# Kernel optimization log

Measured on AMD Instinct MI355X. Metric: run time of the kernel, lower is better.

## Reference

```python
import jax, jax.numpy as jnp
import numpy as np
import math

B, T, N, D, L, H, TE = 4, 1024, 1024, 1024, 512, 16, 1024
HD = D // H  # 64


def layer_norm(x, g, b, eps=1e-5):
    m = jnp.mean(x, axis=-1, keepdims=True)
    v = jnp.var(x, axis=-1, keepdims=True)
    return (x - m) * jax.lax.rsqrt(v + eps) * g + b


def setup_inputs() -> dict:
    key = jax.random.key(0)
    ks = jax.random.split(key, 16)
    s = 0.02
    return {
        "x": jax.random.normal(ks[0], (B, T, D), jnp.float32),
        "xf": jax.random.normal(ks[1], (B, N, L), jnp.float32),
        "emb": jax.random.normal(ks[2], (B, TE), jnp.float32),
        "src_mask": jnp.ones((B, T, N), jnp.float32),
        # LayerNorms
        "ln_g": jnp.ones((D,), jnp.float32), "ln_b": jnp.zeros((D,), jnp.float32),
        "aln_g": jnp.ones((L,), jnp.float32), "aln_b": jnp.zeros((L,), jnp.float32),
        "n2_g": jnp.ones((D,), jnp.float32), "n2_b": jnp.zeros((D,), jnp.float32),
        # Q/K/V projections
        "Wq": jax.random.normal(ks[3], (D, D), jnp.float32) * s,
        "bq": jnp.zeros((D,), jnp.float32),
        "Wk": jax.random.normal(ks[4], (L, D), jnp.float32) * s,
        "bk": jnp.zeros((D,), jnp.float32),
        "Wv": jax.random.normal(ks[5], (L, D), jnp.float32) * s,
        "bv": jnp.zeros((D,), jnp.float32),
        # AdaLN: emb_layers Linear(TE, 2D); out Linear(D, D) (random, not zeroed, to exercise grads)
        "emb_W": jax.random.normal(ks[6], (TE, 2 * D), jnp.float32) * s,
        "emb_b": jnp.zeros((2 * D,), jnp.float32),
        "out_W": jax.random.normal(ks[7], (D, D), jnp.float32) * s,
        "out_b": jnp.zeros((D,), jnp.float32),
    }


def reference(x, xf, emb, src_mask, ln_g, ln_b, aln_g, aln_b, n2_g, n2_b,
              Wq, bq, Wk, bk, Wv, bv, emb_W, emb_b, out_W, out_b):
    xn = layer_norm(x, ln_g, ln_b)                      # B,T,D
    xfn = layer_norm(xf, aln_g, aln_b)                  # B,N,L
    q = (xn @ Wq + bq).reshape(B, T, H, HD)
    k = (xfn @ Wk + bk).reshape(B, N, H, HD)
    v = (xfn @ Wv + bv).reshape(B, N, H, HD)
    # scores: B,T,N,H; scaled by sqrt(head_dim)
    scores = jnp.einsum('bthd,bnhd->btnh', q, k) / math.sqrt(HD)
    scores = scores + (1.0 - src_mask[..., None]) * -100000.0
    weight = jax.nn.softmax(scores, axis=2)             # softmax over N
    y = jnp.einsum('btnh,bnhd->bthd', weight, v).reshape(B, T, D)
    # AdaLN proj_out
    emb_out = (jax.nn.silu(emb) @ emb_W + emb_b)[:, None, :]  # B,1,2D
    scale, shift = jnp.split(emb_out, 2, axis=2)
    h = layer_norm(y, n2_g, n2_b) * (1.0 + scale) + shift
    h = jax.nn.silu(h) @ out_W + out_b
    return x + h
```

## Files before the change

kernel.cpp:

```cpp
#include <hip/hip_runtime.h>

typedef __bf16 bf16;
typedef __bf16 bf16x4 __attribute__((ext_vector_type(4)));
typedef __bf16 bf16x8 __attribute__((ext_vector_type(8)));
typedef float f32x4 __attribute__((ext_vector_type(4)));

#define AS1C(p) ((const __attribute__((address_space(1))) void*)(p))
#define AS3(p)  ((__attribute__((address_space(3))) void*)(p))

__global__ __launch_bounds__(256) void transpose_cast(
    const float* __restrict__ in, bf16* __restrict__ out, int R, int C)
{
    __shared__ float tile[32][33];
    int tx = threadIdx.x & 31, ty = threadIdx.x >> 5;
    int r0 = blockIdx.y * 32, c0 = blockIdx.x * 32;
#pragma unroll
    for (int i = 0; i < 32; i += 8)
        tile[ty + i][tx] = in[(long)(r0 + ty + i) * C + c0 + tx];
    __syncthreads();
#pragma unroll
    for (int i = 0; i < 32; i += 8)
        out[(long)(c0 + ty + i) * R + r0 + tx] = (bf16)tile[tx][ty + i];
}

__global__ __launch_bounds__(256) void concat_bias(
    const float* __restrict__ b0, const float* __restrict__ b1, float* __restrict__ o)
{
    int c = blockIdx.x * 256 + threadIdx.x;
    o[c] = (c < 1024) ? b0[c] : b1[c - 1024];
}

template<int DIM, int NT>
__global__ __launch_bounds__(NT) void ln_to_bf16(
    const float* __restrict__ in, const float* __restrict__ g,
    const float* __restrict__ bb, bf16* __restrict__ out)
{
    constexpr int NW = NT / 64;
    long row = blockIdx.x;
    const float4* x4 = (const float4*)(in + row * DIM);
    float4 v = x4[threadIdx.x];
    float s = v.x + v.y + v.z + v.w;
    float s2 = v.x*v.x + v.y*v.y + v.z*v.z + v.w*v.w;
#pragma unroll
    for (int o = 32; o; o >>= 1) { s += __shfl_xor(s, o); s2 += __shfl_xor(s2, o); }
    __shared__ float red[2][NW];
    int w = threadIdx.x >> 6;
    if ((threadIdx.x & 63) == 0) { red[0][w] = s; red[1][w] = s2; }
    __syncthreads();
    s = 0.f; s2 = 0.f;
#pragma unroll
    for (int i = 0; i < NW; ++i) { s += red[0][i]; s2 += red[1][i]; }
    float mean = s * (1.f / DIM);
    float rstd = rsqrtf(s2 * (1.f / DIM) - mean * mean + 1e-5f);
    int c = threadIdx.x * 4;
    float4 gg = *(const float4*)(g + c);
    float4 bv = *(const float4*)(bb + c);
    bf16x4 ov;
    ov[0] = (bf16)((v.x - mean) * rstd * gg.x + bv.x);
    ov[1] = (bf16)((v.y - mean) * rstd * gg.y + bv.y);
    ov[2] = (bf16)((v.z - mean) * rstd * gg.z + bv.z);
    ov[3] = (bf16)((v.w - mean) * rstd * gg.w + bv.w);
    *(bf16x4*)(out + row * DIM + c) = ov;
}

__global__ __launch_bounds__(256) void mask_flags(
    const float* __restrict__ mask, unsigned char* __restrict__ flags)
{
    int blk = blockIdx.x;
    int b = blk >> 8, qt = (blk >> 4) & 15, kt = blk & 15;
    const float* src = mask + ((long)(b * 1024 + qt * 64 + (threadIdx.x >> 2))) * 1024
                     + kt * 64 + (threadIdx.x & 3) * 16;
    int ok = 1;
#pragma unroll
    for (int u = 0; u < 16; u += 4) {
        float4 v = *(const float4*)(src + u);
        ok &= (v.x == 1.f) & (v.y == 1.f) & (v.z == 1.f) & (v.w == 1.f);
    }
    ok = __syncthreads_and(ok);
    if (threadIdx.x == 0) flags[blk] = (unsigned char)ok;
}

__global__ __launch_bounds__(256) void adaln_gemm2(
    const float* __restrict__ emb, const float* __restrict__ W,
    const float* __restrict__ eb, float* __restrict__ emo)
{
    __shared__ float es[1024];
    __shared__ float part[4][64];
    int b = blockIdx.y, t = threadIdx.x;
    int kg = t >> 6, c = t & 63;
    int col = blockIdx.x * 64 + c;
    for (int i = t; i < 1024; i += 256) {
        float e = emb[b * 1024 + i];
        es[i] = e / (1.f + expf(-e));
    }
    __syncthreads();
    float acc = 0.f;
    const float* wp = W + (long)(kg * 256) * 2048 + col;
    const float* ep = es + kg * 256;
#pragma unroll 4
    for (int k = 0; k < 256; ++k) acc += ep[k] * wp[(long)k * 2048];
    part[kg][c] = acc;
    __syncthreads();
    if (t < 64) {
        int col0 = blockIdx.x * 64 + t;
        emo[b * 2048 + col0] = part[0][t] + part[1][t] + part[2][t] + part[3][t] + eb[col0];
    }
}

template<int OUT_MODE>
__global__ __launch_bounds__(256) void gemm64(
    const bf16* __restrict__ A, const bf16* __restrict__ Bt,
    const float* __restrict__ bias, const float* __restrict__ resid,
    void* __restrict__ outp, int M, int N, int K)
{
    __shared__ __align__(16) bf16 As[64 * 32];
    __shared__ __align__(16) bf16 Bs[128 * 32];
    const int t = threadIdx.x;
    const int wave = t >> 6, lane = t & 63;
    const int brow = blockIdx.y * 64, bcol = blockIdx.x * 128;
    const int wr = wave & 1, wc = wave >> 1;
    const int sr = lane >> 2, sc8 = (lane & 3) * 8;
    const bf16* aS  = A  + (long)(brow + wave * 16 + sr) * K + sc8;
    const bf16* bS0 = Bt + (long)(bcol + wave * 32 + sr) * K + sc8;
    const bf16* bS1 = bS0 + (long)16 * K;
    char* asw = (char*)As + wave * 1024;
    char* bsw = (char*)Bs + wave * 2048;
    const int fr = lane & 15, fc = (lane >> 4) * 8;
    f32x4 acc[2][4] = {};
    for (int k0 = 0; k0 < K; k0 += 32) {
        __syncthreads();
        __builtin_amdgcn_global_load_lds(AS1C(aS + k0),  AS3(asw), 16, 0, 0);
        __builtin_amdgcn_global_load_lds(AS1C(bS0 + k0), AS3(bsw), 16, 0, 0);
        __builtin_amdgcn_global_load_lds(AS1C(bS1 + k0), AS3(bsw + 1024), 16, 0, 0);
        __syncthreads();
        bf16x8 af[2], bfr[4];
#pragma unroll
        for (int m = 0; m < 2; ++m)
            af[m] = *(const bf16x8*)&As[(wr * 32 + m * 16 + fr) * 32 + fc];
#pragma unroll
        for (int n = 0; n < 4; ++n)
            bfr[n] = *(const bf16x8*)&Bs[(wc * 64 + n * 16 + fr) * 32 + fc];
        __builtin_amdgcn_s_setprio(1);
#pragma unroll
        for (int m = 0; m < 2; ++m)
#pragma unroll
            for (int n = 0; n < 4; ++n)
                acc[m][n] = __builtin_amdgcn_mfma_f32_16x16x32_bf16(af[m], bfr[n], acc[m][n], 0, 0, 0);
        __builtin_amdgcn_s_setprio(0);
    }
    const int er = (lane >> 4) * 4, ec = lane & 15;
    if constexpr (OUT_MODE == 0) {
        bf16* C = (bf16*)outp;
#pragma unroll
        for (int n = 0; n < 4; ++n) {
            int col = bcol + wc * 64 + n * 16 + ec;
            float bcv = bias[col];
#pragma unroll
            for (int m = 0; m < 2; ++m) {
                long rbase = (long)(brow + wr * 32 + m * 16 + er) * N + col;
#pragma unroll
                for (int j = 0; j < 4; ++j)
                    C[rbase + (long)j * N] = (bf16)(acc[m][n][j] + bcv);
            }
        }
    } else {
        float* C = (float*)outp;
#pragma unroll
        for (int n = 0; n < 4; ++n) {
            int col = bcol + wc * 64 + n * 16 + ec;
            float bcv = bias[col];
#pragma unroll
            for (int m = 0; m < 2; ++m) {
                long rbase = (long)(brow + wr * 32 + m * 16 + er) * N + col;
#pragma unroll
                for (int j = 0; j < 4; ++j) {
                    long idx = rbase + (long)j * N;
                    C[idx] = resid[idx] + acc[m][n][j] + bcv;
                }
            }
        }
    }
}

__global__ __launch_bounds__(256) void vtrans(
    const bf16* __restrict__ kvb, bf16* __restrict__ vt)
{
    __shared__ bf16 tile[64 * 72];
    int kvt = blockIdx.x, bh = blockIdx.y;
    int b = bh >> 4, h = bh & 15;
    int t = threadIdx.x;
    {
        int key = t >> 2, d0 = (t & 3) * 16;
        const bf16* src = kvb + (long)(b * 1024 + kvt * 64 + key) * 2048 + 1024 + h * 64 + d0;
        bf16x8 v0 = *(const bf16x8*)src;
        bf16x8 v1 = *(const bf16x8*)(src + 8);
        *(bf16x8*)&tile[key * 72 + d0] = v0;
        *(bf16x8*)&tile[key * 72 + d0 + 8] = v1;
    }
    __syncthreads();
    bf16* vtile = vt + ((long)(bh * 16 + kvt)) * 4096;
    int d = t >> 2;
    int phi = (d & 3) | (((d >> 3) & 1) << 2);
#pragma unroll
    for (int half = 0; half < 2; ++half) {
        int c = (t & 3) + half * 4;
        int key8 = 8 * (c ^ phi);
        bf16x8 w;
#pragma unroll
        for (int j = 0; j < 8; ++j) w[j] = tile[(key8 + j) * 72 + d];
        *(bf16x8*)&vtile[d * 64 + c * 8] = w;
    }
}

__global__ __launch_bounds__(256, 4) void flash2(
    const bf16* __restrict__ Q, const bf16* __restrict__ KV, const bf16* __restrict__ VT,
    const float* __restrict__ mask, const unsigned char* __restrict__ flags,
    bf16* __restrict__ Y)
{
    const int f = blockIdx.x;
    const int bh = f & 63;
    const int qt = f >> 6;
    const int b = bh >> 4, h = bh & 15;
    const int t = threadIdx.x, wave = t >> 6, lane = t & 63;
    const int la = lane >> 4, lb = lane & 15;

    __shared__ __align__(16) bf16 Ks[64 * 64];
    __shared__ __align__(16) bf16 Vs[64 * 64];

    const int qrow = qt * 64 + wave * 16;
    bf16x8 qf0, qf1;
    {
        const bf16* qp = Q + (long)(b * 1024 + qrow + lb) * 1024 + h * 64 + la * 8;
        qf0 = *(const bf16x8*)qp;
        qf1 = *(const bf16x8*)(qp + 32);
    }
    f32x4 o[4] = {};
    float m_run = -3e38f, l_run = 0.f;
    const float CL = 0.125f * 1.44269504f;

    const int srow = lane >> 3, sc = lane & 7;
    const int phiS = (srow & 3) | ((wave & 1) << 2);
    const bf16* kS = KV + (long)(b * 1024 + wave * 8 + srow) * 2048 + h * 64 + ((sc ^ phiS) * 8);
    const bf16* vS = VT + (long)(bh * 16) * 4096 + wave * 512 + lane * 8;
    char* kDst = (char*)Ks + wave * 1024;
    char* vDst = (char*)Vs + wave * 1024;

    const int phiK = (lb & 3) | (((lb >> 2) & 1) << 2);
    const int phiV = (lb & 3) | (((lb >> 3) & 1) << 2);
    const int rbase = (lb >> 2) * 8 + (lb & 3);
    const bf16* kf0 = &Ks[rbase * 64 + ((la ^ phiK) * 8)];
    const bf16* kf1 = &Ks[rbase * 64 + (((4 + la) ^ phiK) * 8)];
    const bf16* vf0 = &Vs[lb * 64 + ((la ^ phiV) * 8)];
    const bf16* vf1 = &Vs[lb * 64 + (((4 + la) ^ phiV) * 8)];
    const int rowoff[4] = {0, 2048, 256, 2304};

    const unsigned char* flagrow = flags + b * 256 + qt * 16;
    const float* mrow_p = mask + (long)(b * 1024 + qrow + lb) * 1024;

    for (int kv = 0; kv < 16; ++kv) {
        const int key0 = kv * 64;
        __syncthreads();
        __builtin_amdgcn_global_load_lds(AS1C(kS + (long)key0 * 2048),        AS3(kDst),        16, 0, 0);
        __builtin_amdgcn_global_load_lds(AS1C(kS + (long)(key0 + 32) * 2048), AS3(kDst + 4096), 16, 0, 0);
        __builtin_amdgcn_global_load_lds(AS1C(vS + kv * 4096),                AS3(vDst),        16, 0, 0);
        __builtin_amdgcn_global_load_lds(AS1C(vS + kv * 4096 + 2048),         AS3(vDst + 4096), 16, 0, 0);
        __syncthreads();

        f32x4 s[4] = {};
        __builtin_amdgcn_s_setprio(1);
#pragma unroll
        for (int n = 0; n < 4; ++n) {
            s[n] = __builtin_amdgcn_mfma_f32_16x16x32_bf16(*(const bf16x8*)(kf0 + rowoff[n]), qf0, s[n], 0, 0, 0);
            s[n] = __builtin_amdgcn_mfma_f32_16x16x32_bf16(*(const bf16x8*)(kf1 + rowoff[n]), qf1, s[n], 0, 0, 0);
        }
        __builtin_amdgcn_s_setprio(0);

        if (!flagrow[kv]) {
#pragma unroll
            for (int n = 0; n < 4; ++n)
#pragma unroll
                for (int r = 0; r < 4; ++r) {
                    int key = (n & 1) * 32 + la * 8 + (n >> 1) * 4 + r;
                    s[n][r] += (1.f - mrow_p[key0 + key]) * -800000.f;
                }
        }

        float t0 = fmaxf(fmaxf(s[0][0], s[0][1]), fmaxf(s[0][2], s[0][3]));
        float t1 = fmaxf(fmaxf(s[1][0], s[1][1]), fmaxf(s[1][2], s[1][3]));
        float t2 = fmaxf(fmaxf(s[2][0], s[2][1]), fmaxf(s[2][2], s[2][3]));
        float t3 = fmaxf(fmaxf(s[3][0], s[3][1]), fmaxf(s[3][2], s[3][3]));
        float tmax = fmaxf(fmaxf(t0, t1), fmaxf(t2, t3));
        tmax = fmaxf(tmax, __shfl_xor(tmax, 16));
        tmax = fmaxf(tmax, __shfl_xor(tmax, 32));
        float mnew = fmaxf(m_run, tmax);
        float al = exp2f((m_run - mnew) * CL);
        m_run = mnew;
        float p[4][4];
        float rsum = 0.f;
#pragma unroll
        for (int n = 0; n < 4; ++n)
#pragma unroll
            for (int r = 0; r < 4; ++r) {
                p[n][r] = exp2f((s[n][r] - mnew) * CL);
                rsum += p[n][r];
            }
        rsum += __shfl_xor(rsum, 16);
        rsum += __shfl_xor(rsum, 32);
        l_run = l_run * al + rsum;
#pragma unroll
        for (int d = 0; d < 4; ++d) o[d] *= al;

        bf16x8 pb0, pb1;
#pragma unroll
        for (int j = 0; j < 4; ++j) {
            pb0[j] = (bf16)p[0][j]; pb0[j + 4] = (bf16)p[2][j];
            pb1[j] = (bf16)p[1][j]; pb1[j + 4] = (bf16)p[3][j];
        }

        __builtin_amdgcn_s_setprio(1);
#pragma unroll
        for (int d = 0; d < 4; ++d) {
            o[d] = __builtin_amdgcn_mfma_f32_16x16x32_bf16(*(const bf16x8*)(vf0 + d * 1024), pb0, o[d], 0, 0, 0);
            o[d] = __builtin_amdgcn_mfma_f32_16x16x32_bf16(*(const bf16x8*)(vf1 + d * 1024), pb1, o[d], 0, 0, 0);
        }
        __builtin_amdgcn_s_setprio(0);
    }

    float inv = 1.f / l_run;
    bf16* yp = Y + (long)(b * 1024 + qrow + lb) * 1024 + h * 64 + la * 4;
#pragma unroll
    for (int d = 0; d < 4; ++d) {
        bf16x4 yv;
#pragma unroll
        for (int j = 0; j < 4; ++j) yv[j] = (bf16)(o[d][j] * inv);
        *(bf16x4*)(yp + d * 16) = yv;
    }
}

__global__ __launch_bounds__(256) void ln_mod_silu(
    const bf16* __restrict__ Yin, const float* __restrict__ g, const float* __restrict__ bb,
    const float* __restrict__ emo, bf16* __restrict__ act)
{
    long row = blockIdx.x;
    int b = (int)(row >> 10);
    const bf16* y = Yin + row * 1024;
    int c = threadIdx.x * 4;
    bf16x4 yv = *(const bf16x4*)(y + c);
    float v0 = (float)yv[0], v1 = (float)yv[1], v2 = (float)yv[2], v3 = (float)yv[3];
    float s = v0 + v1 + v2 + v3, s2 = v0*v0 + v1*v1 + v2*v2 + v3*v3;
#pragma unroll
    for (int o = 32; o; o >>= 1) { s += __shfl_xor(s, o); s2 += __shfl_xor(s2, o); }
    __shared__ float red[2][4];
    int w = threadIdx.x >> 6;
    if ((threadIdx.x & 63) == 0) { red[0][w] = s; red[1][w] = s2; }
    __syncthreads();
    s = red[0][0] + red[0][1] + red[0][2] + red[0][3];
    s2 = red[1][0] + red[1][1] + red[1][2] + red[1][3];
    float mean = s * (1.f / 1024.f);
    float rstd = rsqrtf(s2 * (1.f / 1024.f) - mean * mean + 1e-5f);
    float4 gg = *(const float4*)(g + c);
    float4 bv = *(const float4*)(bb + c);
    float4 scv = *(const float4*)(emo + b * 2048 + c);
    float4 shv = *(const float4*)(emo + b * 2048 + 1024 + c);
    float hv[4];
    hv[0] = ((v0 - mean) * rstd * gg.x + bv.x) * (1.f + scv.x) + shv.x;
    hv[1] = ((v1 - mean) * rstd * gg.y + bv.y) * (1.f + scv.y) + shv.y;
    hv[2] = ((v2 - mean) * rstd * gg.z + bv.z) * (1.f + scv.z) + shv.z;
    hv[3] = ((v3 - mean) * rstd * gg.w + bv.w) * (1.f + scv.w) + shv.w;
    bf16x4 ov;
#pragma unroll
    for (int j = 0; j < 4; ++j) ov[j] = (bf16)(hv[j] / (1.f + expf(-hv[j])));
    *(bf16x4*)(act + row * 1024 + c) = ov;
}

extern "C" void kernel_launch(void* const* d_in, const int* in_sizes, int n_in,
                              void* d_out, int out_size, void* d_ws, size_t ws_size,
                              hipStream_t stream)
{
    const float* x     = (const float*)d_in[0];
    const float* xf    = (const float*)d_in[1];
    const float* emb   = (const float*)d_in[2];
    const float* mask  = (const float*)d_in[3];
    const float* ln_g  = (const float*)d_in[4];
    const float* ln_b  = (const float*)d_in[5];
    const float* aln_g = (const float*)d_in[6];
    const float* aln_b = (const float*)d_in[7];
    const float* n2_g  = (const float*)d_in[8];
    const float* n2_b  = (const float*)d_in[9];
    const float* Wq    = (const float*)d_in[10];
    const float* bq    = (const float*)d_in[11];
    const float* Wk    = (const float*)d_in[12];
    const float* bk    = (const float*)d_in[13];
    const float* Wv    = (const float*)d_in[14];
    const float* bv    = (const float*)d_in[15];
    const float* emb_W = (const float*)d_in[16];
    const float* emb_b = (const float*)d_in[17];
    const float* out_W = (const float*)d_in[18];
    const float* out_b = (const float*)d_in[19];
    float* out = (float*)d_out;

    char* w = (char*)d_ws;
    bf16* xn   = (bf16*)w; w += (size_t)4096 * 1024 * 2;
    bf16* xfn  = (bf16*)w; w += (size_t)4096 * 512 * 2;
    bf16* WqT  = (bf16*)w; w += (size_t)1024 * 1024 * 2;
    bf16* WkvT = (bf16*)w; w += (size_t)2048 * 512 * 2;
    bf16* WoT  = (bf16*)w; w += (size_t)1024 * 1024 * 2;
    bf16* qb   = (bf16*)w; w += (size_t)4096 * 1024 * 2;
    bf16* kvb  = (bf16*)w; w += (size_t)4096 * 2048 * 2;
    bf16* yb   = (bf16*)w; w += (size_t)4096 * 1024 * 2;
    float* bkv = (float*)w; w += (size_t)2048 * 4;
    float* emo = (float*)w; w += (size_t)4 * 2048 * 4;
    unsigned char* flg = (unsigned char*)w;
    bf16* vt   = xn;
    bf16* actb = xn;

    transpose_cast<<<dim3(32, 32), 256, 0, stream>>>(Wq,    WqT, 1024, 1024);
    transpose_cast<<<dim3(32, 16), 256, 0, stream>>>(Wk,    WkvT, 512, 1024);
    transpose_cast<<<dim3(32, 16), 256, 0, stream>>>(Wv,    WkvT + (size_t)1024 * 512, 512, 1024);
    transpose_cast<<<dim3(32, 32), 256, 0, stream>>>(out_W, WoT, 1024, 1024);
    concat_bias<<<8, 256, 0, stream>>>(bk, bv, bkv);

    ln_to_bf16<1024, 256><<<4096, 256, 0, stream>>>(x,  ln_g,  ln_b,  xn);
    ln_to_bf16<512, 128><<<4096, 128, 0, stream>>>(xf, aln_g, aln_b, xfn);
    mask_flags<<<1024, 256, 0, stream>>>(mask, flg);
    adaln_gemm2<<<dim3(32, 4), 256, 0, stream>>>(emb, emb_W, emb_b, emo);

    gemm64<0><<<dim3(8, 64),  256, 0, stream>>>(xn,  WqT,  bq,  nullptr, qb,  4096, 1024, 1024);
    gemm64<0><<<dim3(16, 64), 256, 0, stream>>>(xfn, WkvT, bkv, nullptr, kvb, 4096, 2048, 512);
    vtrans<<<dim3(16, 64), 256, 0, stream>>>(kvb, vt);

    flash2<<<1024, 256, 0, stream>>>(qb, kvb, vt, mask, flg, yb);

    ln_mod_silu<<<4096, 256, 0, stream>>>(yb, n2_g, n2_b, emo, actb);
    gemm64<1><<<dim3(8, 64), 256, 0, stream>>>(actb, WoT, out_b, x, out, 4096, 1024, 1024);
}
```

Measured before the change: 300.0 us.

## Double-buffer GEMM and attention K/V loads, fuse prep and LN launches, lazy rescale

Weight transposes and the bias concat now run as one launch, and the two LayerNorms share a single kernel. The Q and KV projections are combined into one GEMM launch. The GEMM core moves to K-tiles of 64 with an XOR-swizzled LDS layout and double-buffered global_load_lds prefetch, and the flash attention kernel double-buffers its K/V tiles the same way. Attention also skips the online-softmax rescale unless the running max grows by more than a threshold, and it packs the mask flags into a bitmask. These changes aim to cut launch overhead and hide memory latency, at the cost of more LDS use, which may lower occupancy.

```diff
diff --git a/kernel.cpp b/kernel.cpp
--- a/kernel.cpp
+++ b/kernel.cpp
@@ -1,6 +1,7 @@
 #include <hip/hip_runtime.h>
 
 typedef __bf16 bf16;
+typedef __bf16 bf16x2 __attribute__((ext_vector_type(2)));
 typedef __bf16 bf16x4 __attribute__((ext_vector_type(4)));
 typedef __bf16 bf16x8 __attribute__((ext_vector_type(8)));
 typedef float f32x4 __attribute__((ext_vector_type(4)));
@@ -8,12 +9,27 @@
 #define AS1C(p) ((const __attribute__((address_space(1))) void*)(p))
 #define AS3(p)  ((__attribute__((address_space(3))) void*)(p))
 
-__global__ __launch_bounds__(256) void transpose_cast(
-    const float* __restrict__ in, bf16* __restrict__ out, int R, int C)
-{
+__global__ __launch_bounds__(256) void prep(
+    const float* __restrict__ Wq, const float* __restrict__ Wk,
+    const float* __restrict__ Wv, const float* __restrict__ Wo,
+    const float* __restrict__ bk, const float* __restrict__ bv,
+    bf16* __restrict__ WqT, bf16* __restrict__ WkvT, bf16* __restrict__ WoT,
+    float* __restrict__ bkv)
+{
+    int blk = blockIdx.x;
+    if (blk >= 3072) {
+        int c = (blk - 3072) * 256 + threadIdx.x;
+        bkv[c] = (c < 1024) ? bk[c] : bv[c - 1024];
+        return;
+    }
+    const float* in; bf16* out; int R, C, bx, by;
+    if (blk < 1024)      { in = Wq; out = WqT; R = 1024; C = 1024; bx = blk & 31; by = blk >> 5; }
+    else if (blk < 1536) { int g = blk - 1024; in = Wk; out = WkvT; R = 512; C = 1024; bx = g & 31; by = g >> 5; }
+    else if (blk < 2048) { int g = blk - 1536; in = Wv; out = WkvT + (size_t)1024 * 512; R = 512; C = 1024; bx = g & 31; by = g >> 5; }
+    else                 { int g = blk - 2048; in = Wo; out = WoT; R = 1024; C = 1024; bx = g & 31; by = g >> 5; }
     __shared__ float tile[32][33];
     int tx = threadIdx.x & 31, ty = threadIdx.x >> 5;
-    int r0 = blockIdx.y * 32, c0 = blockIdx.x * 32;
+    int r0 = by * 32, c0 = bx * 32;
 #pragma unroll
     for (int i = 0; i < 32; i += 8)
         tile[ty + i][tx] = in[(long)(r0 + ty + i) * C + c0 + tx];
@@ -23,44 +39,59 @@
         out[(long)(c0 + ty + i) * R + r0 + tx] = (bf16)tile[tx][ty + i];
 }
 
-__global__ __launch_bounds__(256) void concat_bias(
-    const float* __restrict__ b0, const float* __restrict__ b1, float* __restrict__ o)
-{
-    int c = blockIdx.x * 256 + threadIdx.x;
-    o[c] = (c < 1024) ? b0[c] : b1[c - 1024];
-}
-
-template<int DIM, int NT>
-__global__ __launch_bounds__(NT) void ln_to_bf16(
-    const float* __restrict__ in, const float* __restrict__ g,
-    const float* __restrict__ bb, bf16* __restrict__ out)
-{
-    constexpr int NW = NT / 64;
+__global__ __launch_bounds__(256) void ln_fused(
+    const float* __restrict__ x, const float* __restrict__ xf,
+    const float* __restrict__ g1, const float* __restrict__ b1,
+    const float* __restrict__ g2, const float* __restrict__ b2,
+    bf16* __restrict__ xn, bf16* __restrict__ xfn)
+{
     long row = blockIdx.x;
-    const float4* x4 = (const float4*)(in + row * DIM);
-    float4 v = x4[threadIdx.x];
-    float s = v.x + v.y + v.z + v.w;
-    float s2 = v.x*v.x + v.y*v.y + v.z*v.z + v.w*v.w;
-#pragma unroll
-    for (int o = 32; o; o >>= 1) { s += __shfl_xor(s, o); s2 += __shfl_xor(s2, o); }
-    __shared__ float red[2][NW];
+    __shared__ float red[2][4];
     int w = threadIdx.x >> 6;
-    if ((threadIdx.x & 63) == 0) { red[0][w] = s; red[1][w] = s2; }
-    __syncthreads();
-    s = 0.f; s2 = 0.f;
-#pragma unroll
-    for (int i = 0; i < NW; ++i) { s += red[0][i]; s2 += red[1][i]; }
-    float mean = s * (1.f / DIM);
-    float rstd = rsqrtf(s2 * (1.f / DIM) - mean * mean + 1e-5f);
-    int c = threadIdx.x * 4;
-    float4 gg = *(const float4*)(g + c);
-    float4 bv = *(const float4*)(bb + c);
-    bf16x4 ov;
-    ov[0] = (bf16)((v.x - mean) * rstd * gg.x + bv.x);
-    ov[1] = (bf16)((v.y - mean) * rstd * gg.y + bv.y);
-    ov[2] = (bf16)((v.z - mean) * rstd * gg.z + bv.z);
-    ov[3] = (bf16)((v.w - mean) * rstd * gg.w + bv.w);
-    *(bf16x4*)(out + row * DIM + c) = ov;
+    if (row < 4096) {
+        const float4* x4 = (const float4*)(x + row * 1024);
+        float4 v = x4[threadIdx.x];
+        float s = v.x + v.y + v.z + v.w;
+        float s2 = v.x*v.x + v.y*v.y + v.z*v.z + v.w*v.w;
+#pragma unroll
+        for (int o = 32; o; o >>= 1) { s += __shfl_xor(s, o); s2 += __shfl_xor(s2, o); }
+        if ((threadIdx.x & 63) == 0) { red[0][w] = s; red[1][w] = s2; }
+        __syncthreads();
+        s = red[0][0] + red[0][1] + red[0][2] + red[0][3];
+        s2 = red[1][0] + red[1][1] + red[1][2] + red[1][3];
+        float mean = s * (1.f / 1024.f);
+        float rstd = rsqrtf(s2 * (1.f / 1024.f) - mean * mean + 1e-5f);
+        int c = threadIdx.x * 4;
+        float4 gg = *(const float4*)(g1 + c);
+        float4 bb = *(const float4*)(b1 + c);
+        bf16x4 ov;
+        ov[0] = (bf16)((v.x - mean) * rstd * gg.x + bb.x);
+        ov[1] = (bf16)((v.y - mean) * rstd * gg.y + bb.y);
+        ov[2] = (bf16)((v.z - mean) * rstd * gg.z + bb.z);
+        ov[3] = (bf16)((v.w - mean) * rstd * gg.w + bb.w);
+        *(bf16x4*)(xn + row * 1024 + c) = ov;
+    } else {
+        long r2 = row - 4096;
+        const float2* x2 = (const float2*)(xf + r2 * 512);
+        float2 v = x2[threadIdx.x];
+        float s = v.x + v.y;
+        float s2 = v.x*v.x + v.y*v.y;
+#pragma unroll
+        for (int o = 32; o; o >>= 1) { s += __shfl_xor(s, o); s2 += __shfl_xor(s2, o); }
+        if ((threadIdx.x & 63) == 0) { red[0][w] = s; red[1][w] = s2; }
+        __syncthreads();
+        s = red[0][0] + red[0][1] + red[0][2] + red[0][3];
+        s2 = red[1][0] + red[1][1] + red[1][2] + red[1][3];
+        float mean = s * (1.f / 512.f);
+        float rstd = rsqrtf(s2 * (1.f / 512.f) - mean * mean + 1e-5f);
+        int c = threadIdx.x * 2;
+        float2 gg = *(const float2*)(g2 + c);
+        float2 bb = *(const float2*)(b2 + c);
+        bf16x2 ov;
+        ov[0] = (bf16)((v.x - mean) * rstd * gg.x + bb.x);
+        ov[1] = (bf16)((v.y - mean) * rstd * gg.y + bb.y);
+        *(bf16x2*)(xfn + r2 * 512 + c) = ov;
+    }
 }
 
 __global__ __launch_bounds__(256) void mask_flags(
@@ -108,47 +139,87 @@
 }
 
 template<int OUT_MODE>
-__global__ __launch_bounds__(256) void gemm64(
+__device__ __forceinline__ void gemm_core(
     const bf16* __restrict__ A, const bf16* __restrict__ Bt,
     const float* __restrict__ bias, const float* __restrict__ resid,
-    void* __restrict__ outp, int M, int N, int K)
-{
-    __shared__ __align__(16) bf16 As[64 * 32];
-    __shared__ __align__(16) bf16 Bs[128 * 32];
+    void* __restrict__ outp, int N, int K, int brow, int bcol,
+    bf16* As, bf16* Bs)
+{
     const int t = threadIdx.x;
     const int wave = t >> 6, lane = t & 63;
-    const int brow = blockIdx.y * 64, bcol = blockIdx.x * 128;
     const int wr = wave & 1, wc = wave >> 1;
-    const int sr = lane >> 2, sc8 = (lane & 3) * 8;
-    const bf16* aS  = A  + (long)(brow + wave * 16 + sr) * K + sc8;
-    const bf16* bS0 = Bt + (long)(bcol + wave * 32 + sr) * K + sc8;
-    const bf16* bS1 = bS0 + (long)16 * K;
-    char* asw = (char*)As + wave * 1024;
-    char* bsw = (char*)Bs + wave * 2048;
-    const int fr = lane & 15, fc = (lane >> 4) * 8;
+    const int l3 = lane >> 3, l7 = lane & 7;
+    const int swz = (l7 ^ (l3 & 7)) * 8;
+    const bf16* aS = A  + (long)(brow + wave * 8 + l3) * K + swz;
+    const bf16* bS = Bt + (long)(bcol + wave * 8 + l3) * K + swz;
+    char* aD = (char*)As + wave * 1024;
+    char* bD = (char*)Bs + wave * 1024;
+    const int fr = lane & 15, la = lane >> 4;
+    int afOff[2][2], bfOff[4][2];
+#pragma unroll
+    for (int m = 0; m < 2; ++m)
+#pragma unroll
+        for (int kk = 0; kk < 2; ++kk)
+            afOff[m][kk] = (wr * 32 + m * 16 + fr) * 64 + (((kk * 4 + la) ^ (fr & 7)) * 8);
+#pragma unroll
+    for (int n = 0; n < 4; ++n)
+#pragma unroll
+        for (int kk = 0; kk < 2; ++kk)
+            bfOff[n][kk] = (wc * 64 + n * 16 + fr) * 64 + (((kk * 4 + la) ^ (fr & 7)) * 8);
+
+    const int nt = K >> 6;
     f32x4 acc[2][4] = {};
-    for (int k0 = 0; k0 < K; k0 += 32) {
-        __syncthreads();
-        __builtin_amdgcn_global_load_lds(AS1C(aS + k0),  AS3(asw), 16, 0, 0);
-        __builtin_amdgcn_global_load_lds(AS1C(bS0 + k0), AS3(bsw), 16, 0, 0);
-        __builtin_amdgcn_global_load_lds(AS1C(bS1 + k0), AS3(bsw + 1024), 16, 0, 0);
-        __syncthreads();
-        bf16x8 af[2], bfr[4];
+
+#define G_STAGE(TI, BSEL) do {                                                       \
+        long k0 = (long)(TI) * 64;                                                   \
+        _Pragma("unroll")                                                            \
+        for (int p = 0; p < 2; ++p)                                                  \
+            __builtin_amdgcn_global_load_lds(AS1C(aS + k0 + (long)p * 32 * K),       \
+                AS3(aD + (BSEL) * 8192 + p * 4096), 16, 0, 0);                       \
+        _Pragma("unroll")                                                            \
+        for (int p = 0; p < 4; ++p)                                                  \
+            __builtin_amdgcn_global_load_lds(AS1C(bS + k0 + (long)p * 32 * K),       \
+                AS3(bD + (BSEL) * 16384 + p * 4096), 16, 0, 0);                      \
+    } while (0)
+
+    G_STAGE(0, 0);
+    int cur = 0;
+    for (int ti = 0; ti < nt; ++ti) {
+        if (ti + 1 < nt) {
+            G_STAGE(ti + 1, cur ^ 1);
+            asm volatile("s_waitcnt vmcnt(6)" ::: "memory");
+        } else {
+            asm volatile("s_waitcnt vmcnt(0)" ::: "memory");
+        }
+        __builtin_amdgcn_s_barrier();
+        const bf16* ab = As + cur * 4096;
+        const bf16* bb = Bs + cur * 8192;
+        bf16x8 af[2][2], bf_[4][2];
 #pragma unroll
         for (int m = 0; m < 2; ++m)
-            af[m] = *(const bf16x8*)&As[(wr * 32 + m * 16 + fr) * 32 + fc];
+#pragma unroll
+            for (int kk = 0; kk < 2; ++kk)
+                af[m][kk] = *(const bf16x8*)&ab[afOff[m][kk]];
 #pragma unroll
         for (int n = 0; n < 4; ++n)
-            bfr[n] = *(const bf16x8*)&Bs[(wc * 64 + n * 16 + fr) * 32 + fc];
+#pragma unroll
+            for (int kk = 0; kk < 2; ++kk)
+                bf_[n][kk] = *(const bf16x8*)&bb[bfOff[n][kk]];
         __builtin_amdgcn_s_setprio(1);
 #pragma unroll
-        for (int m = 0; m < 2; ++m)
-#pragma unroll
-            for (int n = 0; n < 4; ++n)
-                acc[m][n] = __builtin_amdgcn_mfma_f32_16x16x32_bf16(af[m], bfr[n], acc[m][n], 0, 0, 0);
+        for (int kk = 0; kk < 2; ++kk)
+#pragma unroll
+            for (int m = 0; m < 2; ++m)
+#pragma unroll
+                for (int n = 0; n < 4; ++n)
+                    acc[m][n] = __builtin_amdgcn_mfma_f32_16x16x32_bf16(af[m][kk], bf_[n][kk], acc[m][n], 0, 0, 0);
         __builtin_amdgcn_s_setprio(0);
-    }
-    const int er = (lane >> 4) * 4, ec = lane & 15;
+        __builtin_amdgcn_s_barrier();
+        cur ^= 1;
+    }
+#undef G_STAGE
+
+    const int er = la * 4, ec = fr;
     if constexpr (OUT_MODE == 0) {
         bf16* C = (bf16*)outp;
 #pragma unroll
@@ -180,6 +251,34 @@
             }
         }
     }
+}
+
+__global__ __launch_bounds__(256) void qkv_gemm(
+    const bf16* __restrict__ xn, const bf16* __restrict__ WqT, const float* __restrict__ bq,
+    bf16* __restrict__ qb,
+    const bf16* __restrict__ xfn, const bf16* __restrict__ WkvT, const float* __restrict__ bkv,
+    bf16* __restrict__ kvb)
+{
+    __shared__ __align__(16) bf16 As[2 * 4096];
+    __shared__ __align__(16) bf16 Bs[2 * 8192];
+    int f = blockIdx.x;
+    if (f < 512)
+        gemm_core<0>(xn, WqT, bq, nullptr, qb, 1024, 1024, (f >> 3) * 64, (f & 7) * 128, As, Bs);
+    else {
+        int g = f - 512;
+        gemm_core<0>(xfn, WkvT, bkv, nullptr, kvb, 2048, 512, (g >> 4) * 64, (g & 15) * 128, As, Bs);
+    }
+}
+
+template<int OUT_MODE>
+__global__ __launch_bounds__(256) void gemm_dbuf(
+    const bf16* __restrict__ A, const bf16* __restrict__ Bt,
+    const float* __restrict__ bias, const float* __restrict__ resid,
+    void* __restrict__ outp, int N, int K)
+{
+    __shared__ __align__(16) bf16 As[2 * 4096];
+    __shared__ __align__(16) bf16 Bs[2 * 8192];
+    gemm_core<OUT_MODE>(A, Bt, bias, resid, outp, N, K, blockIdx.y * 64, blockIdx.x * 128, As, Bs);
 }
 
 __global__ __launch_bounds__(256) void vtrans(
@@ -212,7 +311,7 @@
     }
 }
 
-__global__ __launch_bounds__(256, 4) void flash2(
+__global__ __launch_bounds__(256, 4) void flash3(
     const bf16* __restrict__ Q, const bf16* __restrict__ KV, const bf16* __restrict__ VT,
     const float* __restrict__ mask, const unsigned char* __restrict__ flags,
     bf16* __restrict__ Y)
@@ -224,8 +323,8 @@
     const int t = threadIdx.x, wave = t >> 6, lane = t & 63;
     const int la = lane >> 4, lb = lane & 15;
 
-    __shared__ __align__(16) bf16 Ks[64 * 64];
-    __shared__ __align__(16) bf16 Vs[64 * 64];
+    __shared__ __align__(16) bf16 Ks[2][64 * 64];
+    __shared__ __align__(16) bf16 Vs[2][64 * 64];
 
     const int qrow = qt * 64 + wave * 16;
     bf16x8 qf0, qf1;
@@ -242,40 +341,62 @@
     const int phiS = (srow & 3) | ((wave & 1) << 2);
     const bf16* kS = KV + (long)(b * 1024 + wave * 8 + srow) * 2048 + h * 64 + ((sc ^ phiS) * 8);
     const bf16* vS = VT + (long)(bh * 16) * 4096 + wave * 512 + lane * 8;
-    char* kDst = (char*)Ks + wave * 1024;
-    char* vDst = (char*)Vs + wave * 1024;
+    char* kD0 = (char*)Ks + wave * 1024;
+    char* vD0 = (char*)Vs + wave * 1024;
 
     const int phiK = (lb & 3) | (((lb >> 2) & 1) << 2);
     const int phiV = (lb & 3) | (((lb >> 3) & 1) << 2);
     const int rbase = (lb >> 2) * 8 + (lb & 3);
-    const bf16* kf0 = &Ks[rbase * 64 + ((la ^ phiK) * 8)];
-    const bf16* kf1 = &Ks[rbase * 64 + (((4 + la) ^ phiK) * 8)];
-    const bf16* vf0 = &Vs[lb * 64 + ((la ^ phiV) * 8)];
-    const bf16* vf1 = &Vs[lb * 64 + (((4 + la) ^ phiV) * 8)];
+    const int kOff0 = rbase * 64 + ((la ^ phiK) * 8);
+    const int kOff1 = rbase * 64 + (((4 + la) ^ phiK) * 8);
+    const int vOff0 = lb * 64 + ((la ^ phiV) * 8);
+    const int vOff1 = lb * 64 + (((4 + la) ^ phiV) * 8);
     const int rowoff[4] = {0, 2048, 256, 2304};
 
     const unsigned char* flagrow = flags + b * 256 + qt * 16;
+    unsigned fl = 0;
+#pragma unroll
+    for (int i = 0; i < 16; ++i) fl |= ((unsigned)flagrow[i]) << i;
     const float* mrow_p = mask + (long)(b * 1024 + qrow + lb) * 1024;
 
+    asm volatile("s_waitcnt vmcnt(0)" ::: "memory");
+
+#define F_STAGE(KVI, BSEL) do {                                                        \
+        const long key0_ = (long)(KVI) * 64;                                           \
+        __builtin_amdgcn_global_load_lds(AS1C(kS + key0_ * 2048),                      \
+            AS3(kD0 + (BSEL) * 8192), 16, 0, 0);                                       \
+        __builtin_amdgcn_global_load_lds(AS1C(kS + (key0_ + 32) * 2048),               \
+            AS3(kD0 + (BSEL) * 8192 + 4096), 16, 0, 0);                                \
+        __builtin_amdgcn_global_load_lds(AS1C(vS + (KVI) * 4096),                      \
+            AS3(vD0 + (BSEL) * 8192), 16, 0, 0);                                       \
+        __builtin_amdgcn_global_load_lds(AS1C(vS + (KVI) * 4096 + 2048),               \
+            AS3(vD0 + (BSEL) * 8192 + 4096), 16, 0, 0);                                \
+    } while (0)
+
+    F_STAGE(0, 0);
+    int cur = 0;
     for (int kv = 0; kv < 16; ++kv) {
-        const int key0 = kv * 64;
-        __syncthreads();
-        __builtin_amdgcn_global_load_lds(AS1C(kS + (long)key0 * 2048),        AS3(kDst),        16, 0, 0);
-        __builtin_amdgcn_global_load_lds(AS1C(kS + (long)(key0 + 32) * 2048), AS3(kDst + 4096), 16, 0, 0);
-        __builtin_amdgcn_global_load_lds(AS1C(vS + kv * 4096),                AS3(vDst),        16, 0, 0);
-        __builtin_amdgcn_global_load_lds(AS1C(vS + kv * 4096 + 2048),         AS3(vDst + 4096), 16, 0, 0);
-        __syncthreads();
+        if (kv < 15) {
+            F_STAGE(kv + 1, cur ^ 1);
+            asm volatile("s_waitcnt vmcnt(4)" ::: "memory");
+        } else {
+            asm volatile("s_waitcnt vmcnt(0)" ::: "memory");
+        }
+        __builtin_amdgcn_s_barrier();
+        const bf16* kb = &Ks[cur][0];
+        const bf16* vb = &Vs[cur][0];
 
         f32x4 s[4] = {};
         __builtin_amdgcn_s_setprio(1);
 #pragma unroll
         for (int n = 0; n < 4; ++n) {
-            s[n] = __builtin_amdgcn_mfma_f32_16x16x32_bf16(*(const bf16x8*)(kf0 + rowoff[n]), qf0, s[n], 0, 0, 0);
-            s[n] = __builtin_amdgcn_mfma_f32_16x16x32_bf16(*(const bf16x8*)(kf1 + rowoff[n]), qf1, s[n], 0, 0, 0);
+            s[n] = __builtin_amdgcn_mfma_f32_16x16x32_bf16(*(const bf16x8*)(kb + kOff0 + rowoff[n]), qf0, s[n], 0, 0, 0);
+            s[n] = __builtin_amdgcn_mfma_f32_16x16x32_bf16(*(const bf16x8*)(kb + kOff1 + rowoff[n]), qf1, s[n], 0, 0, 0);
         }
         __builtin_amdgcn_s_setprio(0);
 
-        if (!flagrow[kv]) {
+        if (!((fl >> kv) & 1)) {
+            const int key0 = kv * 64;
 #pragma unroll
             for (int n = 0; n < 4; ++n)
 #pragma unroll
@@ -292,23 +413,28 @@
         float tmax = fmaxf(fmaxf(t0, t1), fmaxf(t2, t3));
         tmax = fmaxf(tmax, __shfl_xor(tmax, 16));
         tmax = fmaxf(tmax, __shfl_xor(tmax, 32));
-        float mnew = fmaxf(m_run, tmax);
-        float al = exp2f((m_run - mnew) * CL);
-        m_run = mnew;
+        if (!__all(tmax - m_run <= 64.f)) {
+            float mnew = fmaxf(m_run, tmax);
+            float al = exp2f((m_run - mnew) * CL);
+            l_run *= al;
+#pragma unroll
+            for (int d = 0; d < 4; ++d)
+#pragma unroll
+                for (int j = 0; j < 4; ++j) o[d][j] *= al;
+            m_run = mnew;
+        }
         float p[4][4];
         float rsum = 0.f;
 #pragma unroll
         for (int n = 0; n < 4; ++n)
 #pragma unroll
             for (int r = 0; r < 4; ++r) {
-                p[n][r] = exp2f((s[n][r] - mnew) * CL);
+                p[n][r] = exp2f((s[n][r] - m_run) * CL);
                 rsum += p[n][r];
             }
         rsum += __shfl_xor(rsum, 16);
         rsum += __shfl_xor(rsum, 32);
-        l_run = l_run * al + rsum;
-#pragma unroll
-        for (int d = 0; d < 4; ++d) o[d] *= al;
+        l_run += rsum;
 
         bf16x8 pb0, pb1;
 #pragma unroll
@@ -320,11 +446,14 @@
         __builtin_amdgcn_s_setprio(1);
 #pragma unroll
         for (int d = 0; d < 4; ++d) {
-            o[d] = __builtin_amdgcn_mfma_f32_16x16x32_bf16(*(const bf16x8*)(vf0 + d * 1024), pb0, o[d], 0, 0, 0);
-            o[d] = __builtin_amdgcn_mfma_f32_16x16x32_bf16(*(const bf16x8*)(vf1 + d * 1024), pb1, o[d], 0, 0, 0);
+            o[d] = __builtin_amdgcn_mfma_f32_16x16x32_bf16(*(const bf16x8*)(vb + vOff0 + d * 1024), pb0, o[d], 0, 0, 0);
+            o[d] = __builtin_amdgcn_mfma_f32_16x16x32_bf16(*(const bf16x8*)(vb + vOff1 + d * 1024), pb1, o[d], 0, 0, 0);
         }
         __builtin_amdgcn_s_setprio(0);
-    }
+        __builtin_amdgcn_s_barrier();
+        cur ^= 1;
+    }
+#undef F_STAGE
 
     float inv = 1.f / l_run;
     bf16* yp = Y + (long)(b * 1024 + qrow + lb) * 1024 + h * 64 + la * 4;
@@ -414,23 +543,16 @@
     bf16* vt   = xn;
     bf16* actb = xn;
 
-    transpose_cast<<<dim3(32, 32), 256, 0, stream>>>(Wq,    WqT, 1024, 1024);
-    transpose_cast<<<dim3(32, 16), 256, 0, stream>>>(Wk,    WkvT, 512, 1024);
-    transpose_cast<<<dim3(32, 16), 256, 0, stream>>>(Wv,    WkvT + (size_t)1024 * 512, 512, 1024);
-    transpose_cast<<<dim3(32, 32), 256, 0, stream>>>(out_W, WoT, 1024, 1024);
-    concat_bias<<<8, 256, 0, stream>>>(bk, bv, bkv);
-
-    ln_to_bf16<1024, 256><<<4096, 256, 0, stream>>>(x,  ln_g,  ln_b,  xn);
-    ln_to_bf16<512, 128><<<4096, 128, 0, stream>>>(xf, aln_g, aln_b, xfn);
+    prep<<<3080, 256, 0, stream>>>(Wq, Wk, Wv, out_W, bk, bv, WqT, WkvT, WoT, bkv);
+    ln_fused<<<8192, 256, 0, stream>>>(x, xf, ln_g, ln_b, aln_g, aln_b, xn, xfn);
     mask_flags<<<1024, 256, 0, stream>>>(mask, flg);
     adaln_gemm2<<<dim3(32, 4), 256, 0, stream>>>(emb, emb_W, emb_b, emo);
 
-    gemm64<0><<<dim3(8, 64),  256, 0, stream>>>(xn,  WqT,  bq,  nullptr, qb,  4096, 1024, 1024);
-    gemm64<0><<<dim3(16, 64), 256, 0, stream>>>(xfn, WkvT, bkv, nullptr, kvb, 4096, 2048, 512);
+    qkv_gemm<<<1536, 256, 0, stream>>>(xn, WqT, bq, qb, xfn, WkvT, bkv, kvb);
     vtrans<<<dim3(16, 64), 256, 0, stream>>>(kvb, vt);
 
-    flash2<<<1024, 256, 0, stream>>>(qb, kvb, vt, mask, flg, yb);
+    flash3<<<1024, 256, 0, stream>>>(qb, kvb, vt, mask, flg, yb);
 
     ln_mod_silu<<<4096, 256, 0, stream>>>(yb, n2_g, n2_b, emo, actb);
-    gemm64<1><<<dim3(8, 64), 256, 0, stream>>>(actb, WoT, out_b, x, out, 4096, 1024, 1024);
-}
+    gemm_dbuf<1><<<dim3(8, 64), 256, 0, stream>>>(actb, WoT, out_b, x, out, 1024, 1024);
+}
```

Measured after the change: 261.4 us. 1.15x faster.
